# Performance work log

Measured on AMD Instinct MI355X. Metric: run time of the kernel, lower is better.

## Reference

```python
import jax, jax.numpy as jnp
import numpy as np

N_VERTICES = 1_000_000
N_DIM = 128
B = 16384
K = 10

def setup_inputs() -> dict:
    key = jax.random.key(0)
    k1, k2, k3, k4, k5 = jax.random.split(key, 5)
    emb_table = jax.random.normal(k1, (N_VERTICES, N_DIM), dtype=jnp.float32) * 0.01
    pos_v = jax.random.randint(k2, (B,), 0, N_VERTICES)
    pos_u = jax.random.randint(k3, (B,), 0, N_VERTICES)
    neg_v = jax.random.randint(k4, (B, K), 0, N_VERTICES)
    weights = jax.random.uniform(k5, (B,), dtype=jnp.float32)
    return {"pos_v": pos_v, "pos_u": pos_u, "neg_v": neg_v,
            "weights": weights, "emb_table": emb_table}

def reference(pos_v, pos_u, neg_v, weights, emb_table):
    emb_v = emb_table[pos_v]            # [B, d]
    emb_u = emb_table[pos_u]            # [B, d]
    emb_neg_v = emb_table[neg_v]        # [B, K, d]
    # batched dot: [B,K,d] x [B,d] -> [B,K]
    neg_score = jnp.einsum('bkd,bd->bk', emb_neg_v, emb_v)
    neg_score = jax.nn.log_sigmoid(-neg_score).sum(axis=1)   # [B]
    pos_score = jnp.sum(emb_v * emb_u, axis=1)               # [B]
    score = jax.nn.log_sigmoid(pos_score) + neg_score
    return -jnp.sum(weights * score)
```

## Files before the change

### kernel.cpp

```cpp
#include <hip/hip_runtime.h>
#include <math.h>

constexpr int BATCH = 16384;
constexpr int KNEG  = 10;
constexpr int DIM   = 128;
constexpr int ITEMS_PER_BLOCK = 8;
constexpr int NBLOCKS = BATCH / ITEMS_PER_BLOCK;

__device__ __forceinline__ float log_sigmoid(float x) {
    return fminf(x, 0.0f) - log1pf(expf(-fabsf(x)));
}

__global__ __launch_bounds__(256, 4) void line2nd_main(
    const int*   __restrict__ pos_v,
    const int*   __restrict__ pos_u,
    const int*   __restrict__ neg_v,
    const float* __restrict__ weights,
    const float* __restrict__ emb,
    float*       __restrict__ ws)
{
    const int tid  = threadIdx.x;
    const int lane = tid & 31;
    const int item = tid >> 5;
    const int b    = blockIdx.x * ITEMS_PER_BLOCK + item;

    const float4* vrow = (const float4*)(emb + (size_t)pos_v[b] * DIM);
    const float4* urow = (const float4*)(emb + (size_t)pos_u[b] * DIM);
    const float4 v = vrow[lane];
    const float4 u = urow[lane];

    float dots[KNEG + 1];
    dots[KNEG] = v.x * u.x + v.y * u.y + v.z * u.z + v.w * u.w;

    const int base = b * KNEG;
#pragma unroll
    for (int k = 0; k < KNEG; ++k) {
        const float4* nrow = (const float4*)(emb + (size_t)neg_v[base + k] * DIM);
        const float4 n = nrow[lane];
        dots[k] = v.x * n.x + v.y * n.y + v.z * n.z + v.w * n.w;
    }

#pragma unroll
    for (int k = 0; k <= KNEG; ++k) {
#pragma unroll
        for (int off = 16; off; off >>= 1)
            dots[k] += __shfl_down(dots[k], off, 32);
    }

    __shared__ float partial[ITEMS_PER_BLOCK];
    if (lane == 0) {
        float s = log_sigmoid(dots[KNEG]);
#pragma unroll
        for (int k = 0; k < KNEG; ++k)
            s += log_sigmoid(-dots[k]);
        partial[item] = weights[b] * s;
    }
    __syncthreads();

    if (tid == 0) {
        float acc = 0.0f;
#pragma unroll
        for (int i = 0; i < ITEMS_PER_BLOCK; ++i) acc += partial[i];
        ws[blockIdx.x] = acc;
    }
}

__global__ __launch_bounds__(256) void line2nd_reduce(
    const float* __restrict__ ws,
    float*       __restrict__ out)
{
    const int tid = threadIdx.x;
    float acc = 0.0f;
#pragma unroll
    for (int i = 0; i < NBLOCKS / 256; ++i)
        acc += ws[tid + i * 256];

#pragma unroll
    for (int off = 32; off; off >>= 1)
        acc += __shfl_down(acc, off, 64);

    __shared__ float sp[4];
    if ((tid & 63) == 0) sp[tid >> 6] = acc;
    __syncthreads();
    if (tid == 0)
        out[0] = -(sp[0] + sp[1] + sp[2] + sp[3]);
}

extern "C" void kernel_launch(void* const* d_in, const int* in_sizes, int n_in,
                              void* d_out, int out_size, void* d_ws, size_t ws_size,
                              hipStream_t stream) {
    const int*   pos_v   = (const int*)d_in[0];
    const int*   pos_u   = (const int*)d_in[1];
    const int*   neg_v   = (const int*)d_in[2];
    const float* weights = (const float*)d_in[3];
    const float* emb     = (const float*)d_in[4];
    float*       out     = (float*)d_out;
    float*       ws      = (float*)d_ws;

    line2nd_main<<<dim3(NBLOCKS), 256, 0, stream>>>(pos_v, pos_u, neg_v,
                                                    weights, emb, ws);
    line2nd_reduce<<<dim3(1), 256, 0, stream>>>(ws, out);
}
```

Measured before the change: 577.7 us.

## Bucket-sort gather indices by row to localize embedding table reads

Replaces the direct random gather with a pipeline: count lookups per row bucket, scan the counts, scatter (row, slot) pairs into bucket order, gather the rows in that sorted order into a dense staging buffer, then run the dot-product and log-sigmoid compute from that buffer. The aim is to make the reads of the 512 MB embedding table more local so DRAM and TLB access is more efficient. The cost is several extra kernel launches, atomics, and a roughly 100 MB staging buffer that is written and then read back, which adds a lot of memory traffic.

```diff
diff --git a/kernel.cpp b/kernel.cpp
--- a/kernel.cpp
+++ b/kernel.cpp
@@ -1,45 +1,134 @@
 #include <hip/hip_runtime.h>
 #include <math.h>
+#include <stdint.h>
 
 constexpr int BATCH = 16384;
 constexpr int KNEG  = 10;
 constexpr int DIM   = 128;
+constexpr int SLOTS_PER_ITEM = 12;
+constexpr int NPAIR = BATCH * SLOTS_PER_ITEM;
+constexpr int NBUCKET = 2048;
+constexpr int BUCKET_SHIFT = 9;
+
 constexpr int ITEMS_PER_BLOCK = 8;
-constexpr int NBLOCKS = BATCH / ITEMS_PER_BLOCK;
+constexpr int NBLK_COMPUTE = BATCH / ITEMS_PER_BLOCK;
+constexpr int PAIRS_PER_BLOCK = 32;
+constexpr int NBLK_GATHER = NPAIR / PAIRS_PER_BLOCK;
+
+constexpr size_t WS_CNT   = 0;
+constexpr size_t WS_CUR   = 16384;
+constexpr size_t WS_PAIRS = 32768;
+constexpr size_t WS_D     = 2097152;
+constexpr size_t WS_PART  = 102760448;
 
 __device__ __forceinline__ float log_sigmoid(float x) {
     return fminf(x, 0.0f) - log1pf(expf(-fabsf(x)));
 }
 
-__global__ __launch_bounds__(256, 4) void line2nd_main(
-    const int*   __restrict__ pos_v,
-    const int*   __restrict__ pos_u,
-    const int*   __restrict__ neg_v,
-    const float* __restrict__ weights,
-    const float* __restrict__ emb,
-    float*       __restrict__ ws)
-{
+__device__ __forceinline__ int slot_row(int slot,
+                                        const int* __restrict__ pos_v,
+                                        const int* __restrict__ pos_u,
+                                        const int* __restrict__ neg_v) {
+    int item = slot / SLOTS_PER_ITEM;
+    int j    = slot - item * SLOTS_PER_ITEM;
+    if (j < KNEG) return neg_v[item * KNEG + j];
+    return (j == KNEG) ? pos_v[item] : pos_u[item];
+}
+
+__global__ void k0_zero(unsigned int* __restrict__ cnt) {
+    int t = blockIdx.x * blockDim.x + threadIdx.x;
+    if (t < NBUCKET) cnt[t] = 0u;
+}
+
+__global__ __launch_bounds__(256) void k1_count(
+    const int* __restrict__ pos_v, const int* __restrict__ pos_u,
+    const int* __restrict__ neg_v, unsigned int* __restrict__ cnt) {
+    int slot = blockIdx.x * blockDim.x + threadIdx.x;
+    int row  = slot_row(slot, pos_v, pos_u, neg_v);
+    atomicAdd(&cnt[row >> BUCKET_SHIFT], 1u);
+}
+
+__global__ __launch_bounds__(256) void k2_scan(
+    const unsigned int* __restrict__ cnt, unsigned int* __restrict__ cur) {
+    int t = threadIdx.x;
+    unsigned int local[8];
+    unsigned int s = 0;
+#pragma unroll
+    for (int i = 0; i < 8; ++i) { local[i] = cnt[t * 8 + i]; s += local[i]; }
+
+    unsigned int v = s;
+#pragma unroll
+    for (int d = 1; d < 64; d <<= 1) {
+        unsigned int n = __shfl_up(v, d, 64);
+        if ((t & 63) >= d) v += n;
+    }
+    __shared__ unsigned int wsum[4];
+    if ((t & 63) == 63) wsum[t >> 6] = v;
+    __syncthreads();
+    unsigned int woff = 0;
+    for (int w = 0; w < (t >> 6); ++w) woff += wsum[w];
+    unsigned int run = woff + v - s;
+#pragma unroll
+    for (int i = 0; i < 8; ++i) { cur[t * 8 + i] = run; run += local[i]; }
+}
+
+__global__ __launch_bounds__(256) void k3_scatter(
+    const int* __restrict__ pos_v, const int* __restrict__ pos_u,
+    const int* __restrict__ neg_v, unsigned int* __restrict__ cur,
+    uint64_t* __restrict__ pairs) {
+    int slot = blockIdx.x * blockDim.x + threadIdx.x;
+    int row  = slot_row(slot, pos_v, pos_u, neg_v);
+    unsigned int p = atomicAdd(&cur[row >> BUCKET_SHIFT], 1u);
+    pairs[p] = ((uint64_t)(unsigned int)row << 32) | (unsigned int)slot;
+}
+
+__global__ __launch_bounds__(256) void k4_gather(
+    const uint64_t* __restrict__ pairs, const float* __restrict__ emb,
+    float* __restrict__ D) {
+    int bid = blockIdx.x;
+    constexpr int q = NBLK_GATHER / 8;
+    int swz = (bid % 8) * q + bid / 8;
+    int lane = threadIdx.x & 31;
+    int grp  = threadIdx.x >> 5;
+    int base = swz * PAIRS_PER_BLOCK;
+
+    float4 r[4];
+    uint32_t slot[4];
+#pragma unroll
+    for (int i = 0; i < 4; ++i) {
+        uint64_t p = pairs[base + grp + i * 8];
+        slot[i] = (uint32_t)p;
+        const float4* src = (const float4*)(emb + (size_t)(p >> 32) * DIM);
+        r[i] = src[lane];
+    }
+#pragma unroll
+    for (int i = 0; i < 4; ++i) {
+        float4* dst = (float4*)(D + (size_t)slot[i] * DIM);
+        dst[lane] = r[i];
+    }
+}
+
+__global__ __launch_bounds__(256, 4) void k5_compute(
+    const float* __restrict__ D, const float* __restrict__ weights,
+    float* __restrict__ partials) {
     const int tid  = threadIdx.x;
     const int lane = tid & 31;
     const int item = tid >> 5;
     const int b    = blockIdx.x * ITEMS_PER_BLOCK + item;
+    const size_t sbase = (size_t)b * SLOTS_PER_ITEM * DIM;
 
-    const float4* vrow = (const float4*)(emb + (size_t)pos_v[b] * DIM);
-    const float4* urow = (const float4*)(emb + (size_t)pos_u[b] * DIM);
+    const float4* vrow = (const float4*)(D + sbase + (size_t)KNEG * DIM);
+    const float4* urow = (const float4*)(D + sbase + (size_t)(KNEG + 1) * DIM);
     const float4 v = vrow[lane];
     const float4 u = urow[lane];
 
     float dots[KNEG + 1];
     dots[KNEG] = v.x * u.x + v.y * u.y + v.z * u.z + v.w * u.w;
-
-    const int base = b * KNEG;
 #pragma unroll
     for (int k = 0; k < KNEG; ++k) {
-        const float4* nrow = (const float4*)(emb + (size_t)neg_v[base + k] * DIM);
-        const float4 n = nrow[lane];
+        const float4 n = ((const float4*)(D + sbase + (size_t)k * DIM))[lane];
         dots[k] = v.x * n.x + v.y * n.y + v.z * n.z + v.w * n.w;
     }
-
 #pragma unroll
     for (int k = 0; k <= KNEG; ++k) {
 #pragma unroll
@@ -56,29 +145,24 @@
         partial[item] = weights[b] * s;
     }
     __syncthreads();
-
     if (tid == 0) {
         float acc = 0.0f;
 #pragma unroll
         for (int i = 0; i < ITEMS_PER_BLOCK; ++i) acc += partial[i];
-        ws[blockIdx.x] = acc;
+        partials[blockIdx.x] = acc;
     }
 }
 
-__global__ __launch_bounds__(256) void line2nd_reduce(
-    const float* __restrict__ ws,
-    float*       __restrict__ out)
-{
+__global__ __launch_bounds__(256) void k6_reduce(
+    const float* __restrict__ partials, float* __restrict__ out) {
     const int tid = threadIdx.x;
     float acc = 0.0f;
 #pragma unroll
-    for (int i = 0; i < NBLOCKS / 256; ++i)
-        acc += ws[tid + i * 256];
-
+    for (int i = 0; i < NBLK_COMPUTE / 256; ++i)
+        acc += partials[tid + i * 256];
 #pragma unroll
     for (int off = 32; off; off >>= 1)
         acc += __shfl_down(acc, off, 64);
-
     __shared__ float sp[4];
     if ((tid & 63) == 0) sp[tid >> 6] = acc;
     __syncthreads();
@@ -95,9 +179,19 @@
     const float* weights = (const float*)d_in[3];
     const float* emb     = (const float*)d_in[4];
     float*       out     = (float*)d_out;
-    float*       ws      = (float*)d_ws;
+    char*        ws      = (char*)d_ws;
 
-    line2nd_main<<<dim3(NBLOCKS), 256, 0, stream>>>(pos_v, pos_u, neg_v,
-                                                    weights, emb, ws);
-    line2nd_reduce<<<dim3(1), 256, 0, stream>>>(ws, out);
+    unsigned int* cnt   = (unsigned int*)(ws + WS_CNT);
+    unsigned int* cur   = (unsigned int*)(ws + WS_CUR);
+    uint64_t*     pairs = (uint64_t*)(ws + WS_PAIRS);
+    float*        D     = (float*)(ws + WS_D);
+    float*        part  = (float*)(ws + WS_PART);
+
+    k0_zero   <<<dim3((NBUCKET + 255) / 256), 256, 0, stream>>>(cnt);
+    k1_count  <<<dim3(NPAIR / 256), 256, 0, stream>>>(pos_v, pos_u, neg_v, cnt);
+    k2_scan   <<<dim3(1), 256, 0, stream>>>(cnt, cur);
+    k3_scatter<<<dim3(NPAIR / 256), 256, 0, stream>>>(pos_v, pos_u, neg_v, cur, pairs);
+    k4_gather <<<dim3(NBLK_GATHER), 256, 0, stream>>>(pairs, emb, D);
+    k5_compute<<<dim3(NBLK_COMPUTE), 256, 0, stream>>>(D, weights, part);
+    k6_reduce <<<dim3(1), 256, 0, stream>>>(part, out);
 }
```

After: 669.0 us. 15.8% more time.
